# Performance work log

Hardware: AMD Instinct MI355X
Metric: run time of the kernel (lower is better)

The kernel has to match this reference:

```python
import jax, jax.numpy as jnp
import numpy as np

N, T, D, H = 6144, 3072, 128, 4
ALPHA = 0.2
NEG = -9e15


def mhgat(x, mask, W, a_src, a_dst, fc_W, fc_b):
    # x: [n, D], mask: [n, n] (0/1), W: [H, D, D], a_src/a_dst: [H, D]
    Wh = jnp.einsum('nd,hde->hne', x, W)                      # [H, n, D]
    f_s = jnp.einsum('hne,he->hn', Wh, a_src)                 # [H, n]
    f_d = jnp.einsum('hne,he->hn', Wh, a_dst)                 # [H, n]
    e = jax.nn.leaky_relu(f_s[:, :, None] + f_d[:, None, :], ALPHA)  # [H, n, n]
    scores = jnp.where(mask[None, :, :] > 0, e, NEG)
    attn = jax.nn.softmax(scores, axis=-1)                    # masked softmax over neighbors
    h = jnp.einsum('hnm,hme->hne', attn, Wh)                  # [H, n, D]
    h = jax.nn.elu(h)                                         # concat=True -> elu per head
    h = jnp.transpose(h, (1, 0, 2)).reshape(x.shape[0], H * h.shape[-1])  # [n, H*D]
    return jax.nn.relu(h @ fc_W + fc_b)                       # fully_connectedLyer = Linear+ReLU


def setup_inputs() -> dict:
    key = jax.random.key(0)
    ks = jax.random.split(key, 20)
    s = 0.05
    return {
        'x': jax.random.normal(ks[0], (N, D), jnp.float32),
        'adj': jax.random.randint(ks[1], (N, N), 0, 2, jnp.int32),
        't_x': jax.random.normal(ks[2], (T, D), jnp.float32),
        't_adj': jax.random.randint(ks[3], (T, T), 0, 2, jnp.int32),
        'tfidf_x': jax.random.uniform(ks[4], (T, N), jnp.float32),
        # concept-graph MHGAT params
        'Wg': jax.random.normal(ks[5], (H, D, D), jnp.float32) * s,
        'ag_src': jax.random.normal(ks[6], (H, D), jnp.float32) * s,
        'ag_dst': jax.random.normal(ks[7], (H, D), jnp.float32) * s,
        'fcg_W': jax.random.normal(ks[8], (H * D, D), jnp.float32) * s,
        'fcg_b': jnp.zeros((D,), jnp.float32),
        # text-graph MHGAT params
        'Wt': jax.random.normal(ks[9], (H, D, D), jnp.float32) * s,
        'at_src': jax.random.normal(ks[10], (H, D), jnp.float32) * s,
        'at_dst': jax.random.normal(ks[11], (H, D), jnp.float32) * s,
        'fct_W': jax.random.normal(ks[12], (H * D, D), jnp.float32) * s,
        'fct_b': jnp.zeros((D,), jnp.float32),
        # fusion fc params
        'fus_W': jax.random.normal(ks[13], (D, D), jnp.float32) * s,
        'fus_b': jnp.zeros((D,), jnp.float32),
    }


def reference(x, adj, t_x, t_adj, tfidf_x,
              Wg, ag_src, ag_dst, fcg_W, fcg_b,
              Wt, at_src, at_dst, fct_W, fct_b,
              fus_W, fus_b):
    concept = mhgat(x, adj, Wg, ag_src, ag_dst, fcg_W, fcg_b)        # [N, D]
    gat_text = mhgat(t_x, t_adj, Wt, at_src, at_dst, fct_W, fct_b)   # [T, D]
    c_text = tfidf_x.T @ gat_text                                    # [N, D]
    z = jax.nn.sigmoid(concept + c_text)
    fusion = z * concept + (1.0 - z) * c_text
    return jax.nn.relu(fusion @ fus_W + fus_b)
```

## Files before the change

kernel.cpp:

```cpp
#include <hip/hip_runtime.h>
#include <hip/hip_bf16.h>
#include <stdint.h>

#define N_  6144
#define T_  3072
#define D_  128
#define H_  4
#define HD_ 512

typedef float f32x4 __attribute__((ext_vector_type(4)));
typedef _Float16 f16x8 __attribute__((ext_vector_type(8)));
typedef _Float16 h16x4 __attribute__((ext_vector_type(4)));

#define GLL16(g, s) __builtin_amdgcn_global_load_lds( \
    (const __attribute__((address_space(1))) unsigned int*)(g), \
    (__attribute__((address_space(3))) unsigned int*)(s), 16, 0, 0)

static __device__ __forceinline__ short f2h(float f) {
  union { _Float16 h; short s; } u;
  u.h = (_Float16)f;
  return u.s;
}
static __device__ __forceinline__ unsigned pk2(float f) {
  union { _Float16 h[2]; unsigned u; } t;
  t.h[0] = (_Float16)f; t.h[1] = t.h[0];
  return t.u;
}
static __device__ __forceinline__ unsigned pkmul(unsigned a, unsigned b) {
  unsigned r;
  asm("v_pk_mul_f16 %0, %1, %2" : "=v"(r) : "v"(a), "v"(b));
  return r;
}
static __device__ __forceinline__ unsigned pkmax(unsigned a, unsigned b) {
  unsigned r;
  asm("v_pk_max_f16 %0, %1, %2" : "=v"(r) : "v"(a), "v"(b));
  return r;
}

__global__ __launch_bounds__(256) void bits8_kernel(const int* __restrict__ a0,
                                                    const int* __restrict__ a1,
                                                    unsigned long long* __restrict__ b0,
                                                    unsigned long long* __restrict__ b1,
                                                    int nw0, int nw1) {
  int lane = threadIdx.x & 63;
  int gw = (blockIdx.x * blockDim.x + threadIdx.x) >> 6;
  int nw = (gridDim.x * blockDim.x) >> 6;
  int total8 = (nw0 + nw1) >> 3;
  for (int g = gw; g < total8; g += nw) {
    int w = g * 8;
    const int* src; unsigned long long* dst; long wi;
    if (w < nw0) { src = a0; dst = b0; wi = w; }
    else         { src = a1; dst = b1; wi = w - nw0; }
    int v[8];
#pragma unroll
    for (int j = 0; j < 8; ++j) v[j] = src[(wi + j) * 64 + lane];
    unsigned long long bb[8];
#pragma unroll
    for (int j = 0; j < 8; ++j) bb[j] = __ballot(v[j] != 0);
    if (lane == 0) {
      ulonglong2 s01 = {bb[0], bb[1]}, s23 = {bb[2], bb[3]};
      ulonglong2 s45 = {bb[4], bb[5]}, s67 = {bb[6], bb[7]};
      *(ulonglong2*)(dst + wi + 0) = s01;
      *(ulonglong2*)(dst + wi + 2) = s23;
      *(ulonglong2*)(dst + wi + 4) = s45;
      *(ulonglong2*)(dst + wi + 6) = s67;
    }
  }
}

__global__ __launch_bounds__(256) void cvt2_kernel(const float* __restrict__ in0,
                                                   short* __restrict__ out0,
                                                   const float* __restrict__ in1,
                                                   short* __restrict__ out1,
                                                   int c0, int c1) {
  int i = blockIdx.x * blockDim.x + threadIdx.x;
  const float* in; short* out; long ii;
  if (i < c0) { in = in0; out = out0; ii = i; }
  else if (i < c0 + c1) { in = in1; out = out1; ii = i - c0; }
  else return;
  float4 v = *(const float4*)(in + ii * 4);
  short4 o;
  o.x = f2h(v.x); o.y = f2h(v.y); o.z = f2h(v.z); o.w = f2h(v.w);
  *(short4*)(out + ii * 4) = o;
}

__global__ __launch_bounds__(256) void tcvt2_kernel(const float* __restrict__ in0,
                                                    short* __restrict__ out0,
                                                    const float* __restrict__ in1,
                                                    short* __restrict__ out1,
                                                    int R, int C, long sIn, long sOut,
                                                    int zsplit) {
  __shared__ float t[32][33];
  const float* in; short* out;
  int z = blockIdx.z;
  if (z < zsplit) { in = in0 + (long)z * sIn; out = out0 + (long)z * sOut; }
  else            { in = in1 + (long)(z - zsplit) * sIn; out = out1 + (long)(z - zsplit) * sOut; }
  int c0 = blockIdx.x * 32, r0 = blockIdx.y * 32;
  int tx = threadIdx.x, ty = threadIdx.y;
#pragma unroll
  for (int i = 0; i < 4; ++i)
    t[ty + 8 * i][tx] = in[(long)(r0 + ty + 8 * i) * C + c0 + tx];
  __syncthreads();
#pragma unroll
  for (int i = 0; i < 4; ++i)
    out[(long)(c0 + ty + 8 * i) * R + r0 + tx] = f2h(t[tx][ty + 8 * i]);
}

__global__ __launch_bounds__(256) void fvec2_kernel(const float* __restrict__ x0,
                                                    const float* __restrict__ W0,
                                                    const float* __restrict__ as0,
                                                    const float* __restrict__ ad0,
                                                    float* __restrict__ ea0, float* __restrict__ ec0,
                                                    short* __restrict__ eb0, short* __restrict__ ed0,
                                                    int n0, int xsplit,
                                                    const float* __restrict__ x1,
                                                    const float* __restrict__ W1,
                                                    const float* __restrict__ as1,
                                                    const float* __restrict__ ad1,
                                                    float* __restrict__ ea1, float* __restrict__ ec1,
                                                    short* __restrict__ eb1, short* __restrict__ ed1,
                                                    int n1) {
  const float *x, *W, *a_s, *a_d;
  float *ea, *ec; short *ebh, *edh; int n; long bx;
  if ((int)blockIdx.x < xsplit) { x=x0; W=W0; a_s=as0; a_d=ad0; ea=ea0; ec=ec0; ebh=eb0; edh=ed0; n=n0; bx=blockIdx.x; }
  else { x=x1; W=W1; a_s=as1; a_d=ad1; ea=ea1; ec=ec1; ebh=eb1; edh=ed1; n=n1; bx=blockIdx.x - xsplit; }
  __shared__ float usl[128], udl[128], asl[128], adl[128];
  long idx = bx * 256 + threadIdx.x;
  int h = (int)(idx / n), i = (int)(idx % n);
  int tid = threadIdx.x;
  if (tid < 128) {
    asl[tid] = a_s[h * D_ + tid];
    adl[tid] = a_d[h * D_ + tid];
  }
  __syncthreads();
  {
    int d = tid & 127;
    const float* wr = W + ((long)h * D_ + d) * D_;
    const float* av = (tid < 128) ? asl : adl;
    float s = 0.f;
#pragma unroll 8
    for (int e = 0; e < D_; ++e) s += wr[e] * av[e];
    if (tid < 128) usl[d] = s; else udl[d] = s;
  }
  __syncthreads();
  const float4* xr = (const float4*)(x + (long)i * D_);
  float s = 0.f, t = 0.f;
#pragma unroll 8
  for (int e4 = 0; e4 < 32; ++e4) {
    float4 xv = xr[e4];
    s += xv.x * usl[4 * e4] + xv.y * usl[4 * e4 + 1] + xv.z * usl[4 * e4 + 2] + xv.w * usl[4 * e4 + 3];
    t += xv.x * udl[4 * e4] + xv.y * udl[4 * e4 + 1] + xv.z * udl[4 * e4 + 2] + xv.w * udl[4 * e4 + 3];
  }
  const float L2E = 1.4426950408889634f;
  float fs = s * L2E, fd = t * L2E;
  ea[idx]  = exp2f(fs);
  ec[idx]  = exp2f(0.2f * fs);
  ebh[idx] = f2h(exp2f(fd));
  edh[idx] = f2h(exp2f(0.2f * fd));
}

#define GEMM_BODY(A, BT, K, lda, ldb, outF, outB, ldo, epi, sOutOff)            \
  {                                                                             \
    __shared__ __align__(16) short bs[3][4096];                                 \
    int tid = threadIdx.x, w = tid >> 6, l = tid & 63, lm = l & 15, lg = l >> 4;\
    int row0 = blockIdx.x * 64 + w * 16;                                        \
    int col0 = blockIdx.y * 128;                                                \
    const short* arow = (A) + (long)(row0 + lm) * (lda) + 8 * lg;               \
    const short* bsrc = (BT) + (long)(col0 + 16 * (2 * w) + lm) * (ldb) + 8 * lg;\
    f32x4 acc[8] = {};                                                          \
    int nt = (K) / 32;                                                          \
    f16x8 af = *(const f16x8*)(arow);                                           \
    GLL16(bsrc, &bs[0][(2 * w) * 512]);                                         \
    GLL16(bsrc + 16 * (ldb), &bs[0][(2 * w + 1) * 512]);                        \
    GLL16(bsrc + 32, &bs[1][(2 * w) * 512]);                                    \
    GLL16(bsrc + 32 + 16 * (ldb), &bs[1][(2 * w + 1) * 512]);                   \
    for (int kt = 0; kt < nt; ++kt) {                                           \
      int cur = kt % 3;                                                         \
      int kb = (kt + 1 < nt ? kt + 1 : kt) * 32;                                \
      f16x8 an = *(const f16x8*)(arow + kb);                                    \
      asm volatile("s_waitcnt vmcnt(3)" ::: "memory");                          \
      __builtin_amdgcn_sched_barrier(0);                                        \
      __builtin_amdgcn_s_barrier();                                             \
      __builtin_amdgcn_sched_barrier(0);                                        \
      _Pragma("unroll")                                                         \
      for (int f = 0; f < 8; ++f) {                                             \
        f16x8 bf = *(const f16x8*)(&bs[cur][f * 512 + l * 8]);                  \
        acc[f] = __builtin_amdgcn_mfma_f32_16x16x32_f16(af, bf, acc[f], 0, 0, 0);\
      }                                                                         \
      {                                                                         \
        int kg = (kt + 2 < nt ? kt + 2 : nt - 1) * 32;                          \
        int tb = (kt + 2) % 3;                                                  \
        GLL16(bsrc + kg, &bs[tb][(2 * w) * 512]);                               \
        GLL16(bsrc + kg + 16 * (ldb), &bs[tb][(2 * w + 1) * 512]);              \
      }                                                                         \
      __builtin_amdgcn_sched_barrier(0);                                        \
      af = an;                                                                  \
    }                                                                           \
    _Pragma("unroll")                                                           \
    for (int f = 0; f < 8; ++f) {                                               \
      int col = col0 + 16 * f + lm;                                             \
      _Pragma("unroll")                                                         \
      for (int r = 0; r < 4; ++r) {                                             \
        int row = row0 + 4 * lg + r;                                            \
        if ((epi) == 0) (outB)[(sOutOff) + (long)row * (ldo) + col] = f2h(acc[f][r]); \
        else            (outF)[(sOutOff) + (long)row * (ldo) + col] = acc[f][r];\
      }                                                                         \
    }                                                                           \
  }

__global__ __launch_bounds__(256) void gemm_kernel(const short* __restrict__ A,
                                                   const short* __restrict__ BT,
                                                   int K, int lda, int ldb,
                                                   float* __restrict__ outF, short* __restrict__ outB,
                                                   int ldo, int epi,
                                                   long sA, long sBT, long sOut) {
  int bz = blockIdx.z;
  const short* Ab = A + bz * sA;
  const short* Bb = BT + bz * sBT;
  long oOff = bz * sOut;
  GEMM_BODY(Ab, Bb, K, lda, ldb, outF, outB, ldo, epi, oOff)
}

__global__ __launch_bounds__(256) void gemm2_kernel(const short* __restrict__ A0,
                                                    const short* __restrict__ BT0,
                                                    float* __restrict__ oF0, short* __restrict__ oB0,
                                                    int ldo0, long sOut0, int xlim0, int ylim0,
                                                    const short* __restrict__ A1,
                                                    const short* __restrict__ BT1,
                                                    float* __restrict__ oF1, short* __restrict__ oB1,
                                                    int ldo1, long sOut1, int xlim1, int ylim1,
                                                    int K, int lda, int ldb, int epi,
                                                    long sA, long sBT, int zsplit) {
  int z = blockIdx.z;
  const short *A, *BT; float* outF; short* outB; int ldo; long sOut; int bz;
  if (z < zsplit) {
    if ((int)blockIdx.x >= xlim0 || (int)blockIdx.y >= ylim0) return;
    A = A0; BT = BT0; outF = oF0; outB = oB0; ldo = ldo0; sOut = sOut0; bz = z;
  } else {
    if ((int)blockIdx.x >= xlim1 || (int)blockIdx.y >= ylim1) return;
    A = A1; BT = BT1; outF = oF1; outB = oB1; ldo = ldo1; sOut = sOut1; bz = z - zsplit;
  }
  const short* Ab = A + bz * sA;
  const short* Bb = BT + bz * sBT;
  long oOff = bz * sOut;
  GEMM_BODY(Ab, Bb, K, lda, ldb, outF, outB, ldo, epi, oOff)
}

__global__ __launch_bounds__(256) void reduce_kernel(const float* __restrict__ P,
                                                     int S, long sP,
                                                     const float* __restrict__ bias,
                                                     short* __restrict__ outB,
                                                     int ldo) {
  __shared__ short sm[128][68];
  int tid = threadIdx.x;
  int r0 = blockIdx.x * 64;
#pragma unroll
  for (int k = 0; k < 8; ++k) {
    int e = tid * 4 + k * 1024;
    int row = e >> 7, col = e & 127;
    f32x4 v = {};
    for (int s = 0; s < S; ++s)
      v += *(const f32x4*)(P + (long)s * sP + (long)(r0 + row) * 128 + col);
    const float4 bv = *(const float4*)(bias + col);
    v[0] += bv.x; v[1] += bv.y; v[2] += bv.z; v[3] += bv.w;
#pragma unroll
    for (int q = 0; q < 4; ++q) v[q] = v[q] > 0.f ? v[q] : 0.f;
    sm[col + 0][row] = f2h(v[0]);
    sm[col + 1][row] = f2h(v[1]);
    sm[col + 2][row] = f2h(v[2]);
    sm[col + 3][row] = f2h(v[3]);
  }
  __syncthreads();
  int d = tid >> 1, seg = tid & 1;
  short* dst = outB + (long)d * ldo + r0 + seg * 32;
#pragma unroll
  for (int q = 0; q < 8; ++q) {
    short4 o;
    o.x = sm[d][seg * 32 + 4 * q + 0];
    o.y = sm[d][seg * 32 + 4 * q + 1];
    o.z = sm[d][seg * 32 + 4 * q + 2];
    o.w = sm[d][seg * 32 + 4 * q + 3];
    *(short4*)(dst + 4 * q) = o;
  }
}

__global__ __launch_bounds__(256) void attn2_kernel(const short* __restrict__ WhT0,
                                                    const unsigned char* __restrict__ bits0,
                                                    const float* __restrict__ ea0A,
                                                    const float* __restrict__ ec0A,
                                                    const short* __restrict__ eb0A,
                                                    const short* __restrict__ ed0A,
                                                    _Float16* __restrict__ pacc0,
                                                    float* __restrict__ pz0,
                                                    int n0, int S0, int RB0,
                                                    const short* __restrict__ WhT1,
                                                    const unsigned char* __restrict__ bits1,
                                                    const float* __restrict__ ea1A,
                                                    const float* __restrict__ ec1A,
                                                    const short* __restrict__ eb1A,
                                                    const short* __restrict__ ed1A,
                                                    _Float16* __restrict__ pacc1,
                                                    float* __restrict__ pz1,
                                                    int n1, int S1, int RB1) {
  int z = blockIdx.z;
  const short* WhT; const unsigned char* bits;
  const float *eaA, *ecA; const short *ebA, *edA;
  _Float16* pacc; float* pz; int n, S, RB, sp;
  if (z < S0) {
    WhT = WhT0; bits = bits0; eaA = ea0A; ecA = ec0A; ebA = eb0A; edA = ed0A;
    pacc = pacc0; pz = pz0; n = n0; S = S0; RB = RB0; sp = z;
  } else {
    if ((int)blockIdx.x >= RB1) return;
    WhT = WhT1; bits = bits1; eaA = ea1A; ecA = ec1A; ebA = eb1A; edA = ed1A;
    pacc = pacc1; pz = pz1; n = n1; S = S1; RB = RB1; sp = z - S0;
  }
  int h = blockIdx.y;
  int klen = n / S, k0 = sp * klen;
  const short* whT = WhT + (long)h * D_ * n;
  const short* ebp = ebA + (long)h * n;
  const short* edp = edA + (long)h * n;
  __shared__ __align__(16) short bs[3][4096];
  int tid = threadIdx.x, w = tid >> 6, l = tid & 63, lm = l & 15, lg = l >> 4;
  int i0 = blockIdx.x * 128;
  int r0 = i0 + 32 * w + lm;
  int r1 = r0 + 16;
  unsigned ea0p = pk2(eaA[(long)h * n + r0]), ea1p = pk2(eaA[(long)h * n + r1]);
  unsigned ec0p = pk2(ecA[(long)h * n + r0]), ec1p = pk2(ecA[(long)h * n + r1]);
  const unsigned char* brow0 = bits + (long)r0 * (n >> 3);
  const unsigned char* brow1 = bits + (long)r1 * (n >> 3);
  const short* bsrc = whT + (long)(16 * (2 * w) + lm) * n + 8 * lg + k0;
  f32x4 acc0[8] = {}, acc1[8] = {};
  f32x4 az0 = {}, az1 = {};
  f16x8 ones;
#pragma unroll
  for (int j = 0; j < 8; ++j) ones[j] = (_Float16)1.0f;
  int nt = klen / 32;
  unsigned ebR[4], edR[4], ebS[4], edS[4];
  unsigned m0A, m1A, m0B, m1B;
  *(uint4*)(ebR) = *(const uint4*)(ebp + k0 + 8 * lg);
  *(uint4*)(edR) = *(const uint4*)(edp + k0 + 8 * lg);
  m0A = (*(const unsigned*)(brow0 + (k0 >> 3))) >> (8 * lg);
  m1A = (*(const unsigned*)(brow1 + (k0 >> 3))) >> (8 * lg);
  GLL16(bsrc, &bs[0][(2 * w) * 512]);
  GLL16(bsrc + 16 * n, &bs[0][(2 * w + 1) * 512]);
  GLL16(bsrc + 32, &bs[1][(2 * w) * 512]);
  GLL16(bsrc + 32 + 16 * n, &bs[1][(2 * w + 1) * 512]);

#define ATTN_STEP(KT, EBC, EDC, M0C, M1C, EBN, EDN, M0N, M1N)                   \
  {                                                                             \
    int cur = (KT) % 3;                                                         \
    int kb = ((KT) + 1 < nt ? (KT) + 1 : (KT)) * 32;                            \
    *(uint4*)(EBN) = *(const uint4*)(ebp + k0 + kb + 8 * lg);                   \
    *(uint4*)(EDN) = *(const uint4*)(edp + k0 + kb + 8 * lg);                   \
    M0N = (*(const unsigned*)(brow0 + ((k0 + kb) >> 3))) >> (8 * lg);           \
    M1N = (*(const unsigned*)(brow1 + ((k0 + kb) >> 3))) >> (8 * lg);           \
    union { f16x8 v; unsigned u[4]; } af0, af1;                                 \
    _Pragma("unroll")                                                           \
    for (int jj = 0; jj < 4; ++jj) {                                            \
      unsigned pm0 = pkmax(pkmul(ea0p, EBC[jj]), pkmul(ec0p, EDC[jj]));         \
      unsigned pm1 = pkmax(pkmul(ea1p, EBC[jj]), pkmul(ec1p, EDC[jj]));         \
      int ta = ((int)(M0C << (31 - 2 * jj))) >> 31;                             \
      int tb = ((int)(M0C << (30 - 2 * jj))) >> 31;                             \
      af0.u[jj] = pm0 & __builtin_amdgcn_perm((unsigned)tb, (unsigned)ta, 0x07060302u); \
      ta = ((int)(M1C << (31 - 2 * jj))) >> 31;                                 \
      tb = ((int)(M1C << (30 - 2 * jj))) >> 31;                                 \
      af1.u[jj] = pm1 & __builtin_amdgcn_perm((unsigned)tb, (unsigned)ta, 0x07060302u); \
    }                                                                           \
    asm volatile("s_waitcnt vmcnt(6)" ::: "memory");                            \
    __builtin_amdgcn_sched_barrier(0);                                          \
    __builtin_amdgcn_s_barrier();                                               \
    __builtin_amdgcn_sched_barrier(0);                                          \
    _Pragma("unroll")                                                           \
    for (int f = 0; f < 8; ++f) {                                               \
      f16x8 bf = *(const f16x8*)(&bs[cur][f * 512 + l * 8]);                    \
      acc0[f] = __builtin_amdgcn_mfma_f32_16x16x32_f16(af0.v, bf, acc0[f], 0, 0, 0); \
      acc1[f] = __builtin_amdgcn_mfma_f32_16x16x32_f16(af1.v, bf, acc1[f], 0, 0, 0); \
    }                                                                           \
    az0 = __builtin_amdgcn_mfma_f32_16x16x32_f16(af0.v, ones, az0, 0, 0, 0);    \
    az1 = __builtin_amdgcn_mfma_f32_16x16x32_f16(af1.v, ones, az1, 0, 0, 0);    \
    {                                                                           \
      int kg = ((KT) + 2 < nt ? (KT) + 2 : nt - 1) * 32;                        \
      int tb2 = ((KT) + 2) % 3;                                                 \
      GLL16(bsrc + kg, &bs[tb2][(2 * w) * 512]);                                \
      GLL16(bsrc + kg + 16 * n, &bs[tb2][(2 * w + 1) * 512]);                   \
    }                                                                           \
    __builtin_amdgcn_sched_barrier(0);                                          \
  }

  for (int kt = 0; kt < nt; kt += 2) {
    ATTN_STEP(kt,     ebR, edR, m0A, m1A, ebS, edS, m0B, m1B);
    ATTN_STEP(kt + 1, ebS, edS, m0B, m1B, ebR, edR, m0A, m1A);
  }
#undef ATTN_STEP

  long base = (long)(h * RB + blockIdx.x) * S + sp;
  if (lm == 0) {
#pragma unroll
    for (int r = 0; r < 4; ++r) {
      pz[base * 128 + 32 * w + 4 * lg + r] = az0[r];
      pz[base * 128 + 32 * w + 16 + 4 * lg + r] = az1[r];
    }
  }
  long pb = base * 16384;
#pragma unroll
  for (int f = 0; f < 8; ++f)
#pragma unroll
    for (int r = 0; r < 4; ++r) {
      pacc[pb + (long)(32 * w + 4 * lg + r) * 128 + 16 * f + lm] = (_Float16)acc0[f][r];
      pacc[pb + (long)(32 * w + 16 + 4 * lg + r) * 128 + 16 * f + lm] = (_Float16)acc1[f][r];
    }
}

__global__ __launch_bounds__(256) void combine2_kernel(const _Float16* __restrict__ pacc0,
                                                       const float* __restrict__ pz0,
                                                       short* __restrict__ hcat0,
                                                       int S0, int RB0,
                                                       const _Float16* __restrict__ pacc1,
                                                       const float* __restrict__ pz1,
                                                       short* __restrict__ hcat1,
                                                       int S1) {
  const _Float16* pacc; const float* pz; short* hcat; int S, RB, rb;
  if ((int)blockIdx.x < RB0) { pacc = pacc0; pz = pz0; hcat = hcat0; S = S0; RB = RB0; rb = blockIdx.x; }
  else { pacc = pacc1; pz = pz1; hcat = hcat1; S = S1; RB = gridDim.x - RB0; rb = blockIdx.x - RB0; }
  int h = blockIdx.y;
  long base = (long)(h * RB + rb) * S;
  __shared__ float zl[128];
  int tid = threadIdx.x;
  if (tid < 128) {
    float zv = 0.f;
    for (int s = 0; s < S; ++s) zv += pz[(base + s) * 128 + tid];
    zl[tid] = 1.f / zv;
  }
  __syncthreads();
  int i0 = rb * 128;
#pragma unroll
  for (int k = 0; k < 16; ++k) {
    int e = tid * 4 + k * 1024;
    int row = e >> 7, col = e & 127;
    f32x4 v = {};
    for (int s = 0; s < S; ++s) {
      h16x4 hv = *(const h16x4*)(pacc + (base + s) * 16384 + e);
      v[0] += (float)hv[0]; v[1] += (float)hv[1];
      v[2] += (float)hv[2]; v[3] += (float)hv[3];
    }
    float iz = zl[row];
    short4 o;
    float t;
    t = v[0] * iz; o.x = f2h(t > 0.f ? t : __expf(t) - 1.f);
    t = v[1] * iz; o.y = f2h(t > 0.f ? t : __expf(t) - 1.f);
    t = v[2] * iz; o.z = f2h(t > 0.f ? t : __expf(t) - 1.f);
    t = v[3] * iz; o.w = f2h(t > 0.f ? t : __expf(t) - 1.f);
    *(short4*)(hcat + (long)(i0 + row) * HD_ + h * D_ + col) = o;
  }
}

__global__ __launch_bounds__(256) void fusion_kernel(const float* __restrict__ fcPg,
                                                     int Sf, long sPg,
                                                     const float* __restrict__ fcg_b,
                                                     const float* __restrict__ ctextP,
                                                     int Sc, long sCt,
                                                     const short* __restrict__ fusT,
                                                     const float* __restrict__ fus_b,
                                                     float* __restrict__ out) {
  __shared__ __align__(16) short als[64 * 136];
  int tid = threadIdx.x;
  int r0 = blockIdx.x * 64;
#pragma unroll
  for (int it = 0; it < 8; ++it) {
    int e = it * 1024 + tid * 4;
    int r = e >> 7, c = e & 127;
    f32x4 cv = {};
    for (int s = 0; s < Sf; ++s)
      cv += *(const f32x4*)(fcPg + (long)s * sPg + (long)(r0 + r) * D_ + c);
    const float4 bv = *(const float4*)(fcg_b + c);
    cv[0] += bv.x; cv[1] += bv.y; cv[2] += bv.z; cv[3] += bv.w;
#pragma unroll
    for (int q = 0; q < 4; ++q) cv[q] = cv[q] > 0.f ? cv[q] : 0.f;
    f32x4 tv = {};
    for (int s = 0; s < Sc; ++s)
      tv += *(const f32x4*)(ctextP + (long)s * sCt + (long)(r0 + r) * D_ + c);
    short4 o;
    {
      float s0 = cv[0] + tv[0]; float z = 1.f / (1.f + __expf(-s0)); o.x = f2h(tv[0] + z * (cv[0] - tv[0]));
      s0 = cv[1] + tv[1]; z = 1.f / (1.f + __expf(-s0)); o.y = f2h(tv[1] + z * (cv[1] - tv[1]));
      s0 = cv[2] + tv[2]; z = 1.f / (1.f + __expf(-s0)); o.z = f2h(tv[2] + z * (cv[2] - tv[2]));
      s0 = cv[3] + tv[3]; z = 1.f / (1.f + __expf(-s0)); o.w = f2h(tv[3] + z * (cv[3] - tv[3]));
    }
    *(short4*)(als + (long)r * 136 + c) = o;
  }
  __syncthreads();
  int w = tid >> 6, l = tid & 63, lm = l & 15, lg = l >> 4;
  f32x4 acc[8] = {};
#pragma unroll
  for (int kt = 0; kt < 4; ++kt) {
    int kb = kt * 32;
    f16x8 af = *(const f16x8*)(als + (16 * w + lm) * 136 + kb + 8 * lg);
#pragma unroll
    for (int f = 0; f < 8; ++f) {
      f16x8 bf = *(const f16x8*)(fusT + (long)(16 * f + lm) * D_ + kb + 8 * lg);
      acc[f] = __builtin_amdgcn_mfma_f32_16x16x32_f16(af, bf, acc[f], 0, 0, 0);
    }
  }
#pragma unroll
  for (int f = 0; f < 8; ++f) {
    int col = 16 * f + lm;
#pragma unroll
    for (int r = 0; r < 4; ++r) {
      float v = acc[f][r] + fus_b[col];
      v = v > 0.f ? v : 0.f;
      out[(long)(r0 + 16 * w + 4 * lg + r) * D_ + col] = v;
    }
  }
}

extern "C" void kernel_launch(void* const* d_in, const int* in_sizes, int n_in,
                              void* d_out, int out_size, void* d_ws, size_t ws_size,
                              hipStream_t stream) {
  (void)in_sizes; (void)n_in; (void)out_size;
  const float* x      = (const float*)d_in[0];
  const int*   adj    = (const int*)d_in[1];
  const float* t_x    = (const float*)d_in[2];
  const int*   t_adj  = (const int*)d_in[3];
  const float* tfidf  = (const float*)d_in[4];
  const float* Wg     = (const float*)d_in[5];
  const float* ag_src = (const float*)d_in[6];
  const float* ag_dst = (const float*)d_in[7];
  const float* fcg_W  = (const float*)d_in[8];
  const float* fcg_b  = (const float*)d_in[9];
  const float* Wt     = (const float*)d_in[10];
  const float* at_src = (const float*)d_in[11];
  const float* at_dst = (const float*)d_in[12];
  const float* fct_W  = (const float*)d_in[13];
  const float* fct_b  = (const float*)d_in[14];
  const float* fus_W  = (const float*)d_in[15];
  const float* fus_b  = (const float*)d_in[16];
  float* out = (float*)d_out;

  char* ws = (char*)d_ws;
  size_t off = 0;
  auto alloc = [&](size_t bytes) -> char* {
    char* p = ws + off;
    off = (off + bytes + 255) & ~(size_t)255;
    return p;
  };
  unsigned long long* bitsG = (unsigned long long*)alloc((size_t)N_ * N_ / 8);
  unsigned long long* bitsT = (unsigned long long*)alloc((size_t)T_ * T_ / 8);
  short* xb     = (short*)alloc((size_t)N_ * D_ * 2);
  short* txb    = (short*)alloc((size_t)T_ * D_ * 2);
  short* WgT    = (short*)alloc((size_t)H_ * D_ * D_ * 2);
  short* WtT    = (short*)alloc((size_t)H_ * D_ * D_ * 2);
  short* fcgT   = (short*)alloc((size_t)HD_ * D_ * 2);
  short* fctT   = (short*)alloc((size_t)HD_ * D_ * 2);
  short* fusT   = (short*)alloc((size_t)D_ * D_ * 2);
  short* tfidfT = (short*)alloc((size_t)N_ * T_ * 2);
  short* WhTg   = (short*)alloc((size_t)H_ * D_ * N_ * 2);
  short* WhTt   = (short*)alloc((size_t)H_ * D_ * T_ * 2);
  float* eaG  = (float*)alloc((size_t)H_ * N_ * 4);
  float* ecG  = (float*)alloc((size_t)H_ * N_ * 4);
  short* ebG  = (short*)alloc((size_t)H_ * N_ * 2);
  short* edG  = (short*)alloc((size_t)H_ * N_ * 2);
  float* eaT  = (float*)alloc((size_t)H_ * T_ * 4);
  float* ecT  = (float*)alloc((size_t)H_ * T_ * 4);
  short* ebT  = (short*)alloc((size_t)H_ * T_ * 2);
  short* edT  = (short*)alloc((size_t)H_ * T_ * 2);
  short* hcatG = (short*)alloc((size_t)N_ * HD_ * 2);
  short* hcatT = (short*)alloc((size_t)T_ * HD_ * 2);
  short* gatT  = (short*)alloc((size_t)D_ * T_ * 2);

  const int RBg = N_ / 128, RBt = T_ / 128;
  const size_t paccG1 = (size_t)H_ * RBg * 16384 * 2;
  const size_t paccT1 = (size_t)H_ * RBt * 16384 * 2;
  const size_t pzG1   = (size_t)H_ * RBg * 128 * 4;
  const size_t pzT1   = (size_t)H_ * RBt * 128 * 4;
  const size_t fcPg1  = (size_t)N_ * D_ * 4;
  const size_t fcPt1  = (size_t)T_ * D_ * 4;
  const size_t ctp1   = (size_t)N_ * D_ * 4;
  size_t rem = (ws_size > off + (1 << 20)) ? (ws_size - off - (1 << 20)) : 0;
  int Sg = 2, St = 2, Sf = 2, Sc = 2;
  size_t need8 = 8 * (paccG1 + pzG1) + 8 * (paccT1 + pzT1) + 4 * fcPg1 + 4 * fcPt1 + 4 * ctp1;
  size_t need4 = 4 * (paccG1 + pzG1) + 4 * (paccT1 + pzT1) + 2 * fcPg1 + 2 * fcPt1 + 2 * ctp1;
  if (rem >= need8)      { Sg = 8; St = 8; Sf = 4; Sc = 4; }
  else if (rem >= need4) { Sg = 4; St = 4; Sf = 2; Sc = 2; }
  _Float16* paccG = (_Float16*)alloc(Sg * paccG1);
  float* pzG   = (float*)alloc(Sg * pzG1);
  _Float16* paccT = (_Float16*)alloc(St * paccT1);
  float* pzT   = (float*)alloc(St * pzT1);
  float* fcPg  = (float*)alloc(Sf * fcPg1);
  float* fcPt  = (float*)alloc(Sf * fcPt1);
  float* ctextP = (float*)alloc(Sc * ctp1);

  bits8_kernel<<<dim3(1536), dim3(256), 0, stream>>>(adj, t_adj, bitsG, bitsT,
                                                     N_ * N_ / 64, T_ * T_ / 64);
  cvt2_kernel<<<dim3((N_ + T_) * D_ / 1024), dim3(256), 0, stream>>>(
      x, xb, t_x, txb, N_ * D_ / 4, T_ * D_ / 4);
  tcvt2_kernel<<<dim3(4, 4, 8), dim3(32, 8), 0, stream>>>(
      Wg, WgT, Wt, WtT, D_, D_, (long)D_ * D_, (long)D_ * D_, 4);
  tcvt2_kernel<<<dim3(4, 16, 2), dim3(32, 8), 0, stream>>>(
      fcg_W, fcgT, fct_W, fctT, HD_, D_, 0, 0, 1);
  tcvt2_kernel<<<dim3(4, 4, 1), dim3(32, 8), 0, stream>>>(
      fus_W, fusT, fus_W, fusT, D_, D_, 0, 0, 1);
  tcvt2_kernel<<<dim3(N_ / 32, T_ / 32, 1), dim3(32, 8), 0, stream>>>(
      tfidf, tfidfT, tfidf, tfidfT, T_, N_, 0, 0, 1);
  fvec2_kernel<<<dim3(H_ * N_ / 256 + H_ * T_ / 256), dim3(256), 0, stream>>>(
      x, Wg, ag_src, ag_dst, eaG, ecG, ebG, edG, N_, H_ * N_ / 256,
      t_x, Wt, at_src, at_dst, eaT, ecT, ebT, edT, T_);

  gemm2_kernel<<<dim3(2, N_ / 128, 2 * H_), dim3(256), 0, stream>>>(
      WgT, xb, nullptr, WhTg, N_, (long)D_ * N_, 2, N_ / 128,
      WtT, txb, nullptr, WhTt, T_, (long)D_ * T_, 2, T_ / 128,
      D_, D_, D_, 0, (long)D_ * D_, 0, H_);

  attn2_kernel<<<dim3(RBg, H_, Sg + St), dim3(256), 0, stream>>>(
      WhTg, (const unsigned char*)bitsG, eaG, ecG, ebG, edG, paccG, pzG, N_, Sg, RBg,
      WhTt, (const unsigned char*)bitsT, eaT, ecT, ebT, edT, paccT, pzT, T_, St, RBt);
  combine2_kernel<<<dim3(RBg + RBt, H_), dim3(256), 0, stream>>>(
      paccG, pzG, hcatG, Sg, RBg, paccT, pzT, hcatT, St);

  gemm2_kernel<<<dim3(N_ / 64, 1, 2 * Sf), dim3(256), 0, stream>>>(
      hcatG, fcgT, fcPg, nullptr, D_, (long)N_ * D_, N_ / 64, 1,
      hcatT, fctT, fcPt, nullptr, D_, (long)T_ * D_, T_ / 64, 1,
      HD_ / Sf, HD_, HD_, 3, (long)(HD_ / Sf), (long)(HD_ / Sf), Sf);
  reduce_kernel<<<dim3(T_ / 64), dim3(256), 0, stream>>>(
      fcPt, Sf, (long)T_ * D_, fct_b, gatT, T_);

  gemm_kernel<<<dim3(N_ / 64, 1, Sc), dim3(256), 0, stream>>>(
      tfidfT, gatT, T_ / Sc, T_, T_, ctextP, nullptr, D_, 3,
      (long)(T_ / Sc), (long)(T_ / Sc), (long)N_ * D_);

  fusion_kernel<<<dim3(N_ / 64), dim3(256), 0, stream>>>(
      fcPg, Sf, (long)N_ * D_, fcg_b, ctextP, Sc, (long)N_ * D_, fusT, fus_b, out);
}
```

Measured before the change: 337.9 us.

## Deepen attention K-loop prefetch to four LDS stages with distance three

```diff
diff --git a/kernel.cpp b/kernel.cpp
--- a/kernel.cpp
+++ b/kernel.cpp
@@ -319,7 +319,7 @@
   const short* whT = WhT + (long)h * D_ * n;
   const short* ebp = ebA + (long)h * n;
   const short* edp = edA + (long)h * n;
-  __shared__ __align__(16) short bs[3][4096];
+  __shared__ __align__(16) short bs[4][4096];
   int tid = threadIdx.x, w = tid >> 6, l = tid & 63, lm = l & 15, lg = l >> 4;
   int i0 = blockIdx.x * 128;
   int r0 = i0 + 32 * w + lm;
@@ -335,25 +335,42 @@
 #pragma unroll
   for (int j = 0; j < 8; ++j) ones[j] = (_Float16)1.0f;
   int nt = klen / 32;
-  unsigned ebR[4], edR[4], ebS[4], edS[4];
-  unsigned m0A, m1A, m0B, m1B;
-  *(uint4*)(ebR) = *(const uint4*)(ebp + k0 + 8 * lg);
-  *(uint4*)(edR) = *(const uint4*)(edp + k0 + 8 * lg);
-  m0A = (*(const unsigned*)(brow0 + (k0 >> 3))) >> (8 * lg);
-  m1A = (*(const unsigned*)(brow1 + (k0 >> 3))) >> (8 * lg);
+  unsigned eb0_[4], ed0_[4], eb1_[4], ed1_[4], eb2_[4], ed2_[4], eb3_[4], ed3_[4];
+  unsigned m00, m10, m01, m11, m02, m12, m03, m13;
+  *(uint4*)(eb0_) = *(const uint4*)(ebp + k0 + 8 * lg);
+  *(uint4*)(ed0_) = *(const uint4*)(edp + k0 + 8 * lg);
+  m00 = (*(const unsigned*)(brow0 + (k0 >> 3))) >> (8 * lg);
+  m10 = (*(const unsigned*)(brow1 + (k0 >> 3))) >> (8 * lg);
   GLL16(bsrc, &bs[0][(2 * w) * 512]);
   GLL16(bsrc + 16 * n, &bs[0][(2 * w + 1) * 512]);
+  __builtin_amdgcn_sched_barrier(0);
+  *(uint4*)(eb1_) = *(const uint4*)(ebp + k0 + 32 + 8 * lg);
+  *(uint4*)(ed1_) = *(const uint4*)(edp + k0 + 32 + 8 * lg);
+  m01 = (*(const unsigned*)(brow0 + ((k0 + 32) >> 3))) >> (8 * lg);
+  m11 = (*(const unsigned*)(brow1 + ((k0 + 32) >> 3))) >> (8 * lg);
   GLL16(bsrc + 32, &bs[1][(2 * w) * 512]);
   GLL16(bsrc + 32 + 16 * n, &bs[1][(2 * w + 1) * 512]);
+  __builtin_amdgcn_sched_barrier(0);
+  *(uint4*)(eb2_) = *(const uint4*)(ebp + k0 + 64 + 8 * lg);
+  *(uint4*)(ed2_) = *(const uint4*)(edp + k0 + 64 + 8 * lg);
+  m02 = (*(const unsigned*)(brow0 + ((k0 + 64) >> 3))) >> (8 * lg);
+  m12 = (*(const unsigned*)(brow1 + ((k0 + 64) >> 3))) >> (8 * lg);
+  GLL16(bsrc + 64, &bs[2][(2 * w) * 512]);
+  GLL16(bsrc + 64 + 16 * n, &bs[2][(2 * w + 1) * 512]);
+  __builtin_amdgcn_sched_barrier(0);
 
 #define ATTN_STEP(KT, EBC, EDC, M0C, M1C, EBN, EDN, M0N, M1N)                   \
   {                                                                             \
-    int cur = (KT) % 3;                                                         \
-    int kb = ((KT) + 1 < nt ? (KT) + 1 : (KT)) * 32;                            \
-    *(uint4*)(EBN) = *(const uint4*)(ebp + k0 + kb + 8 * lg);                   \
-    *(uint4*)(EDN) = *(const uint4*)(edp + k0 + kb + 8 * lg);                   \
-    M0N = (*(const unsigned*)(brow0 + ((k0 + kb) >> 3))) >> (8 * lg);           \
-    M1N = (*(const unsigned*)(brow1 + ((k0 + kb) >> 3))) >> (8 * lg);           \
+    int cur = (KT) & 3;                                                         \
+    int tgt = ((KT) + 3) & 3;                                                   \
+    int kpre = ((KT) + 3 < nt ? (KT) + 3 : nt - 1) * 32;                        \
+    *(uint4*)(EBN) = *(const uint4*)(ebp + k0 + kpre + 8 * lg);                 \
+    *(uint4*)(EDN) = *(const uint4*)(edp + k0 + kpre + 8 * lg);                 \
+    M0N = (*(const unsigned*)(brow0 + ((k0 + kpre) >> 3))) >> (8 * lg);         \
+    M1N = (*(const unsigned*)(brow1 + ((k0 + kpre) >> 3))) >> (8 * lg);         \
+    GLL16(bsrc + kpre, &bs[tgt][(2 * w) * 512]);                                \
+    GLL16(bsrc + kpre + 16 * n, &bs[tgt][(2 * w + 1) * 512]);                   \
+    __builtin_amdgcn_sched_barrier(0);                                          \
     union { f16x8 v; unsigned u[4]; } af0, af1;                                 \
     _Pragma("unroll")                                                           \
     for (int jj = 0; jj < 4; ++jj) {                                            \
@@ -366,7 +383,7 @@
       tb = ((int)(M1C << (30 - 2 * jj))) >> 31;                                 \
       af1.u[jj] = pm1 & __builtin_amdgcn_perm((unsigned)tb, (unsigned)ta, 0x07060302u); \
     }                                                                           \
-    asm volatile("s_waitcnt vmcnt(6)" ::: "memory");                            \
+    asm volatile("s_waitcnt vmcnt(18)" ::: "memory");                           \
     __builtin_amdgcn_sched_barrier(0);                                          \
     __builtin_amdgcn_s_barrier();                                               \
     __builtin_amdgcn_sched_barrier(0);                                          \
@@ -378,18 +395,14 @@
     }                                                                           \
     az0 = __builtin_amdgcn_mfma_f32_16x16x32_f16(af0.v, ones, az0, 0, 0, 0);    \
     az1 = __builtin_amdgcn_mfma_f32_16x16x32_f16(af1.v, ones, az1, 0, 0, 0);    \
-    {                                                                           \
-      int kg = ((KT) + 2 < nt ? (KT) + 2 : nt - 1) * 32;                        \
-      int tb2 = ((KT) + 2) % 3;                                                 \
-      GLL16(bsrc + kg, &bs[tb2][(2 * w) * 512]);                                \
-      GLL16(bsrc + kg + 16 * n, &bs[tb2][(2 * w + 1) * 512]);                   \
-    }                                                                           \
     __builtin_amdgcn_sched_barrier(0);                                          \
   }
 
-  for (int kt = 0; kt < nt; kt += 2) {
-    ATTN_STEP(kt,     ebR, edR, m0A, m1A, ebS, edS, m0B, m1B);
-    ATTN_STEP(kt + 1, ebS, edS, m0B, m1B, ebR, edR, m0A, m1A);
+  for (int kt = 0; kt < nt; kt += 4) {
+    ATTN_STEP(kt + 0, eb0_, ed0_, m00, m10, eb3_, ed3_, m03, m13);
+    ATTN_STEP(kt + 1, eb1_, ed1_, m01, m11, eb0_, ed0_, m00, m10);
+    ATTN_STEP(kt + 2, eb2_, ed2_, m02, m12, eb1_, ed1_, m01, m11);
+    ATTN_STEP(kt + 3, eb3_, ed3_, m03, m13, eb2_, ed2_, m02, m12);
   }
 #undef ATTN_STEP
 
```

After: 337.1 us (median of 2 runs). No clear change (-0.2%).

## Double attention row tile per block to 256 rows for B-tile reuse

Applied to the files above, without the earlier changes.

```diff
diff --git a/kernel.cpp b/kernel.cpp
--- a/kernel.cpp
+++ b/kernel.cpp
@@ -321,32 +321,38 @@
   const short* edp = edA + (long)h * n;
   __shared__ __align__(16) short bs[3][4096];
   int tid = threadIdx.x, w = tid >> 6, l = tid & 63, lm = l & 15, lg = l >> 4;
-  int i0 = blockIdx.x * 128;
-  int r0 = i0 + 32 * w + lm;
-  int r1 = r0 + 16;
+  int i0 = blockIdx.x * 256;
+  int rw = i0 + 64 * w;
+  int r0 = rw + lm, r1 = rw + 16 + lm, r2 = rw + 32 + lm, r3 = rw + 48 + lm;
   unsigned ea0p = pk2(eaA[(long)h * n + r0]), ea1p = pk2(eaA[(long)h * n + r1]);
+  unsigned ea2p = pk2(eaA[(long)h * n + r2]), ea3p = pk2(eaA[(long)h * n + r3]);
   unsigned ec0p = pk2(ecA[(long)h * n + r0]), ec1p = pk2(ecA[(long)h * n + r1]);
+  unsigned ec2p = pk2(ecA[(long)h * n + r2]), ec3p = pk2(ecA[(long)h * n + r3]);
   const unsigned char* brow0 = bits + (long)r0 * (n >> 3);
   const unsigned char* brow1 = bits + (long)r1 * (n >> 3);
+  const unsigned char* brow2 = bits + (long)r2 * (n >> 3);
+  const unsigned char* brow3 = bits + (long)r3 * (n >> 3);
   const short* bsrc = whT + (long)(16 * (2 * w) + lm) * n + 8 * lg + k0;
-  f32x4 acc0[8] = {}, acc1[8] = {};
-  f32x4 az0 = {}, az1 = {};
+  f32x4 acc0[8] = {}, acc1[8] = {}, acc2[8] = {}, acc3[8] = {};
+  f32x4 az0 = {}, az1 = {}, az2 = {}, az3 = {};
   f16x8 ones;
 #pragma unroll
   for (int j = 0; j < 8; ++j) ones[j] = (_Float16)1.0f;
   int nt = klen / 32;
   unsigned ebR[4], edR[4], ebS[4], edS[4];
-  unsigned m0A, m1A, m0B, m1B;
+  unsigned m0A, m1A, m2A, m3A, m0B, m1B, m2B, m3B;
   *(uint4*)(ebR) = *(const uint4*)(ebp + k0 + 8 * lg);
   *(uint4*)(edR) = *(const uint4*)(edp + k0 + 8 * lg);
   m0A = (*(const unsigned*)(brow0 + (k0 >> 3))) >> (8 * lg);
   m1A = (*(const unsigned*)(brow1 + (k0 >> 3))) >> (8 * lg);
+  m2A = (*(const unsigned*)(brow2 + (k0 >> 3))) >> (8 * lg);
+  m3A = (*(const unsigned*)(brow3 + (k0 >> 3))) >> (8 * lg);
   GLL16(bsrc, &bs[0][(2 * w) * 512]);
   GLL16(bsrc + 16 * n, &bs[0][(2 * w + 1) * 512]);
   GLL16(bsrc + 32, &bs[1][(2 * w) * 512]);
   GLL16(bsrc + 32 + 16 * n, &bs[1][(2 * w + 1) * 512]);
 
-#define ATTN_STEP(KT, EBC, EDC, M0C, M1C, EBN, EDN, M0N, M1N)                   \
+#define ATTN_STEP(KT, EBC, EDC, M0C, M1C, M2C, M3C, EBN, EDN, M0N, M1N, M2N, M3N) \
   {                                                                             \
     int cur = (KT) % 3;                                                         \
     int kb = ((KT) + 1 < nt ? (KT) + 1 : (KT)) * 32;                            \
@@ -354,19 +360,29 @@
     *(uint4*)(EDN) = *(const uint4*)(edp + k0 + kb + 8 * lg);                   \
     M0N = (*(const unsigned*)(brow0 + ((k0 + kb) >> 3))) >> (8 * lg);           \
     M1N = (*(const unsigned*)(brow1 + ((k0 + kb) >> 3))) >> (8 * lg);           \
-    union { f16x8 v; unsigned u[4]; } af0, af1;                                 \
+    M2N = (*(const unsigned*)(brow2 + ((k0 + kb) >> 3))) >> (8 * lg);           \
+    M3N = (*(const unsigned*)(brow3 + ((k0 + kb) >> 3))) >> (8 * lg);           \
+    union { f16x8 v; unsigned u[4]; } af0, af1, af2, af3;                       \
     _Pragma("unroll")                                                           \
     for (int jj = 0; jj < 4; ++jj) {                                            \
       unsigned pm0 = pkmax(pkmul(ea0p, EBC[jj]), pkmul(ec0p, EDC[jj]));         \
       unsigned pm1 = pkmax(pkmul(ea1p, EBC[jj]), pkmul(ec1p, EDC[jj]));         \
+      unsigned pm2 = pkmax(pkmul(ea2p, EBC[jj]), pkmul(ec2p, EDC[jj]));         \
+      unsigned pm3 = pkmax(pkmul(ea3p, EBC[jj]), pkmul(ec3p, EDC[jj]));         \
       int ta = ((int)(M0C << (31 - 2 * jj))) >> 31;                             \
       int tb = ((int)(M0C << (30 - 2 * jj))) >> 31;                             \
       af0.u[jj] = pm0 & __builtin_amdgcn_perm((unsigned)tb, (unsigned)ta, 0x07060302u); \
       ta = ((int)(M1C << (31 - 2 * jj))) >> 31;                                 \
       tb = ((int)(M1C << (30 - 2 * jj))) >> 31;                                 \
       af1.u[jj] = pm1 & __builtin_amdgcn_perm((unsigned)tb, (unsigned)ta, 0x07060302u); \
+      ta = ((int)(M2C << (31 - 2 * jj))) >> 31;                                 \
+      tb = ((int)(M2C << (30 - 2 * jj))) >> 31;                                 \
+      af2.u[jj] = pm2 & __builtin_amdgcn_perm((unsigned)tb, (unsigned)ta, 0x07060302u); \
+      ta = ((int)(M3C << (31 - 2 * jj))) >> 31;                                 \
+      tb = ((int)(M3C << (30 - 2 * jj))) >> 31;                                 \
+      af3.u[jj] = pm3 & __builtin_amdgcn_perm((unsigned)tb, (unsigned)ta, 0x07060302u); \
     }                                                                           \
-    asm volatile("s_waitcnt vmcnt(6)" ::: "memory");                            \
+    asm volatile("s_waitcnt vmcnt(8)" ::: "memory");                            \
     __builtin_amdgcn_sched_barrier(0);                                          \
     __builtin_amdgcn_s_barrier();                                               \
     __builtin_amdgcn_sched_barrier(0);                                          \
@@ -375,9 +391,13 @@
       f16x8 bf = *(const f16x8*)(&bs[cur][f * 512 + l * 8]);                    \
       acc0[f] = __builtin_amdgcn_mfma_f32_16x16x32_f16(af0.v, bf, acc0[f], 0, 0, 0); \
       acc1[f] = __builtin_amdgcn_mfma_f32_16x16x32_f16(af1.v, bf, acc1[f], 0, 0, 0); \
+      acc2[f] = __builtin_amdgcn_mfma_f32_16x16x32_f16(af2.v, bf, acc2[f], 0, 0, 0); \
+      acc3[f] = __builtin_amdgcn_mfma_f32_16x16x32_f16(af3.v, bf, acc3[f], 0, 0, 0); \
     }                                                                           \
     az0 = __builtin_amdgcn_mfma_f32_16x16x32_f16(af0.v, ones, az0, 0, 0, 0);    \
     az1 = __builtin_amdgcn_mfma_f32_16x16x32_f16(af1.v, ones, az1, 0, 0, 0);    \
+    az2 = __builtin_amdgcn_mfma_f32_16x16x32_f16(af2.v, ones, az2, 0, 0, 0);    \
+    az3 = __builtin_amdgcn_mfma_f32_16x16x32_f16(af3.v, ones, az3, 0, 0, 0);    \
     {                                                                           \
       int kg = ((KT) + 2 < nt ? (KT) + 2 : nt - 1) * 32;                        \
       int tb2 = ((KT) + 2) % 3;                                                 \
@@ -388,8 +408,8 @@
   }
 
   for (int kt = 0; kt < nt; kt += 2) {
-    ATTN_STEP(kt,     ebR, edR, m0A, m1A, ebS, edS, m0B, m1B);
-    ATTN_STEP(kt + 1, ebS, edS, m0B, m1B, ebR, edR, m0A, m1A);
+    ATTN_STEP(kt,     ebR, edR, m0A, m1A, m2A, m3A, ebS, edS, m0B, m1B, m2B, m3B);
+    ATTN_STEP(kt + 1, ebS, edS, m0B, m1B, m2B, m3B, ebR, edR, m0A, m1A, m2A, m3A);
   }
 #undef ATTN_STEP
 
@@ -397,17 +417,21 @@
   if (lm == 0) {
 #pragma unroll
     for (int r = 0; r < 4; ++r) {
-      pz[base * 128 + 32 * w + 4 * lg + r] = az0[r];
-      pz[base * 128 + 32 * w + 16 + 4 * lg + r] = az1[r];
+      pz[base * 256 + 64 * w + 4 * lg + r] = az0[r];
+      pz[base * 256 + 64 * w + 16 + 4 * lg + r] = az1[r];
+      pz[base * 256 + 64 * w + 32 + 4 * lg + r] = az2[r];
+      pz[base * 256 + 64 * w + 48 + 4 * lg + r] = az3[r];
     }
   }
-  long pb = base * 16384;
+  long pb = base * 32768;
 #pragma unroll
   for (int f = 0; f < 8; ++f)
 #pragma unroll
     for (int r = 0; r < 4; ++r) {
-      pacc[pb + (long)(32 * w + 4 * lg + r) * 128 + 16 * f + lm] = (_Float16)acc0[f][r];
-      pacc[pb + (long)(32 * w + 16 + 4 * lg + r) * 128 + 16 * f + lm] = (_Float16)acc1[f][r];
+      pacc[pb + (long)(64 * w + 4 * lg + r) * 128 + 16 * f + lm] = (_Float16)acc0[f][r];
+      pacc[pb + (long)(64 * w + 16 + 4 * lg + r) * 128 + 16 * f + lm] = (_Float16)acc1[f][r];
+      pacc[pb + (long)(64 * w + 32 + 4 * lg + r) * 128 + 16 * f + lm] = (_Float16)acc2[f][r];
+      pacc[pb + (long)(64 * w + 48 + 4 * lg + r) * 128 + 16 * f + lm] = (_Float16)acc3[f][r];
     }
 }
 
@@ -424,22 +448,22 @@
   else { pacc = pacc1; pz = pz1; hcat = hcat1; S = S1; RB = gridDim.x - RB0; rb = blockIdx.x - RB0; }
   int h = blockIdx.y;
   long base = (long)(h * RB + rb) * S;
-  __shared__ float zl[128];
+  __shared__ float zl[256];
   int tid = threadIdx.x;
-  if (tid < 128) {
+  {
     float zv = 0.f;
-    for (int s = 0; s < S; ++s) zv += pz[(base + s) * 128 + tid];
+    for (int s = 0; s < S; ++s) zv += pz[(base + s) * 256 + tid];
     zl[tid] = 1.f / zv;
   }
   __syncthreads();
-  int i0 = rb * 128;
-#pragma unroll
-  for (int k = 0; k < 16; ++k) {
+  int i0 = rb * 256;
+#pragma unroll
+  for (int k = 0; k < 32; ++k) {
     int e = tid * 4 + k * 1024;
     int row = e >> 7, col = e & 127;
     f32x4 v = {};
     for (int s = 0; s < S; ++s) {
-      h16x4 hv = *(const h16x4*)(pacc + (base + s) * 16384 + e);
+      h16x4 hv = *(const h16x4*)(pacc + (base + s) * 32768 + e);
       v[0] += (float)hv[0]; v[1] += (float)hv[1];
       v[2] += (float)hv[2]; v[3] += (float)hv[3];
     }
@@ -567,11 +591,11 @@
   short* hcatT = (short*)alloc((size_t)T_ * HD_ * 2);
   short* gatT  = (short*)alloc((size_t)D_ * T_ * 2);
 
-  const int RBg = N_ / 128, RBt = T_ / 128;
-  const size_t paccG1 = (size_t)H_ * RBg * 16384 * 2;
-  const size_t paccT1 = (size_t)H_ * RBt * 16384 * 2;
-  const size_t pzG1   = (size_t)H_ * RBg * 128 * 4;
-  const size_t pzT1   = (size_t)H_ * RBt * 128 * 4;
+  const int RBg = N_ / 256, RBt = T_ / 256;
+  const size_t paccG1 = (size_t)H_ * RBg * 32768 * 2;
+  const size_t paccT1 = (size_t)H_ * RBt * 32768 * 2;
+  const size_t pzG1   = (size_t)H_ * RBg * 256 * 4;
+  const size_t pzT1   = (size_t)H_ * RBt * 256 * 4;
   const size_t fcPg1  = (size_t)N_ * D_ * 4;
   const size_t fcPt1  = (size_t)T_ * D_ * 4;
   const size_t ctp1   = (size_t)N_ * D_ * 4;
```

Result: slower. 385.1 us (+14.0%).
